# Performance work log

Measured on AMD Instinct MI355X. Metric: run time of the kernel, lower is better.

Reference implementation:

```python
import jax, jax.numpy as jnp
import numpy as np

NUM_NODES = 50000
NUM_EDGES = 800000
IN_CH = 64
OUT_CH = 64


def setup_inputs() -> dict:
    key = jax.random.key(0)
    k1, k2, k3, k4 = jax.random.split(key, 4)
    x = jax.random.normal(k1, (NUM_NODES, IN_CH), dtype=jnp.float32)
    edge_index = jax.random.randint(k2, (2, NUM_EDGES), 0, NUM_NODES, dtype=jnp.int32)
    W = jax.random.normal(k3, (IN_CH, OUT_CH), dtype=jnp.float32) * 0.05
    b = jax.random.normal(k4, (OUT_CH,), dtype=jnp.float32) * 0.05
    return {"x": x, "edge_index": edge_index, "W": W, "b": b}


def reference(x, edge_index, W, b):
    row, col = edge_index[0], edge_index[1]
    # Stage 1: in-degree of target nodes (math of one-hot sum == segment count)
    deg = jax.ops.segment_sum(jnp.ones_like(col, dtype=jnp.float32), col,
                              num_segments=NUM_NODES)
    deg_inv_sqrt = jnp.where(deg > 0, (deg + 1e-16) ** -0.5, 0.0)
    norm = deg_inv_sqrt[row] * deg_inv_sqrt[col]          # [E]
    # Stage 2+3: gather source features and scale by edge norm
    msg = norm[:, None] * x[row]                          # [E, IN_CH]
    # Stage 4: scatter-sum into target nodes (math of one-hot matmul)
    agg = jax.ops.segment_sum(msg, col, num_segments=NUM_NODES)  # [N, IN_CH]
    # Stage 5+6: linear transform + ReLU
    return jax.nn.relu(agg @ W + b)                       # [N, OUT_CH]
```

## Files before the change

### kernel.cpp

```cpp
#include <hip/hip_runtime.h>
#include <hip/hip_fp16.h>


#define C_CH 64
#define BW   128
#define BSH  7
#define MAXBUK 512
#define BIN_CHUNK 4096
#define NPB  32

__global__ void initcur_kernel(int* __restrict__ bcur, int nbuk, int cap) {
    int i = blockIdx.x * blockDim.x + threadIdx.x;
    if (i < nbuk) bcur[i] = i * cap;
}

__global__ void __launch_bounds__(256)
bin_kernel(const int* __restrict__ row, const int* __restrict__ col,
           int* __restrict__ bcur, unsigned* __restrict__ epk,
           int E, int nbuk, int cap) {
    __shared__ int h[MAXBUK];
    __shared__ int rb[MAXBUK];
    __shared__ unsigned short rank[BIN_CHUNK];
    int tid = threadIdx.x;
    int e0 = blockIdx.x * BIN_CHUNK;
    int cntE = E - e0; if (cntE > BIN_CHUNK) cntE = BIN_CHUNK;

    for (int i = tid; i < nbuk; i += 256) h[i] = 0;
    __syncthreads();

    const int4* col4 = (const int4*)(col + e0);
    const int4* row4 = (const int4*)(row + e0);
    int cnt4 = cntE >> 2;
    for (int i = tid; i < cnt4; i += 256) {
        int4 c = col4[i];
        rank[4*i+0] = (unsigned short)atomicAdd(&h[c.x >> BSH], 1);
        rank[4*i+1] = (unsigned short)atomicAdd(&h[c.y >> BSH], 1);
        rank[4*i+2] = (unsigned short)atomicAdd(&h[c.z >> BSH], 1);
        rank[4*i+3] = (unsigned short)atomicAdd(&h[c.w >> BSH], 1);
    }
    for (int i = (cnt4 << 2) + tid; i < cntE; i += 256)
        rank[i] = (unsigned short)atomicAdd(&h[col[e0 + i] >> BSH], 1);
    __syncthreads();

    for (int i = tid; i < nbuk; i += 256)
        rb[i] = h[i] ? atomicAdd(&bcur[i], h[i]) : 0;
    __syncthreads();

    for (int i = tid; i < cnt4; i += 256) {
        int4 c = col4[i];
        int4 r = row4[i];
        #pragma unroll
        for (int j = 0; j < 4; ++j) {
            int cc = (j == 0) ? c.x : (j == 1) ? c.y : (j == 2) ? c.z : c.w;
            int rr = (j == 0) ? r.x : (j == 1) ? r.y : (j == 2) ? r.z : r.w;
            int bkt = cc >> BSH;
            int pos = rb[bkt] + (int)rank[4*i+j];
            if (pos < (bkt + 1) * cap)
                epk[pos] = ((unsigned)(cc & (BW - 1)) << 16) | (unsigned)rr;
        }
    }
    for (int i = (cnt4 << 2) + tid; i < cntE; i += 256) {
        int cc = col[e0 + i];
        int bkt = cc >> BSH;
        int pos = rb[bkt] + (int)rank[i];
        if (pos < (bkt + 1) * cap)
            epk[pos] = ((unsigned)(cc & (BW - 1)) << 16) | (unsigned)row[e0 + i];
    }
}

__global__ void __launch_bounds__(256)
build_kernel(const unsigned* __restrict__ epk, const int* __restrict__ bcur,
             const float* __restrict__ x,
             int* __restrict__ rs, int* __restrict__ re, float* __restrict__ dis,
             unsigned short* __restrict__ srcs, __half* __restrict__ xsh,
             int N, int cap) {
    __shared__ int cnt[BW];
    __shared__ int sc[BW];
    __shared__ int cur[BW];
    __shared__ float dv[BW];
    __shared__ int tot;
    __shared__ unsigned short sl[4096];
    int tid = threadIdx.x;
    int b   = blockIdx.x;
    int base = b * cap;
    int cb = bcur[b] - base; if (cb > cap) cb = cap;
    int nb0 = b << BSH;
    int nn  = N - nb0; if (nn > BW) nn = BW;

    if (tid < BW) cnt[tid] = 0;
    for (int i = tid; i < cap; i += 256)
        sl[i] = (unsigned short)N;
    __syncthreads();
    for (int i = tid; i < cb; i += 256)
        atomicAdd(&cnt[epk[base + i] >> 16], 1);
    __syncthreads();
    if (tid < BW) sc[tid] = (cnt[tid] + 7) & ~7;
    __syncthreads();
    for (int off = 1; off < BW; off <<= 1) {
        int t = (tid < BW && tid >= off) ? sc[tid - off] : 0;
        __syncthreads();
        if (tid < BW) sc[tid] += t;
        __syncthreads();
    }
    if (tid < BW) {
        int d  = cnt[tid];
        int dp = (d + 7) & ~7;
        int ex = sc[tid] - dp;
        cur[tid] = ex;
        if (tid == BW - 1) tot = sc[tid];
        if (tid < nn) {
            rs[nb0 + tid] = base + ex;
            re[nb0 + tid] = base + ex + d;
            float di = (d > 0) ? rsqrtf((float)d) : 0.0f;
            dis[nb0 + tid] = di;
            dv[tid] = di;
        }
    }
    __syncthreads();
    for (int i = tid; i < cb; i += 256) {
        unsigned p = epk[base + i];
        int pos = atomicAdd(&cur[p >> 16], 1);
        if (pos < cap) sl[pos] = (unsigned short)(p & 0xFFFFu);
    }
    __syncthreads();
    int cbp = tot; if (cbp > cap) cbp = cap;
    for (int i = tid; i < cbp; i += 256)
        srcs[base + i] = sl[i];

    int tot2 = nn * (C_CH / 2);
    const float2* x2 = (const float2*)x;
    __half2* o2 = (__half2*)xsh;
    for (int i = tid; i < tot2; i += 256) {
        int nl = i >> 5;
        int c2 = i & 31;
        long long gi = (long long)(nb0 + nl) * (C_CH / 2) + c2;
        float2 v = x2[gi];
        float dn = dv[nl];
        o2[gi] = __floats2half2_rn(v.x * dn, v.y * dn);
    }
    if (b == 0 && tid < C_CH / 2)
        o2[(long long)N * (C_CH / 2) + tid] = __floats2half2_rn(0.0f, 0.0f);
}

__global__ void __launch_bounds__(512)
gather_kernel(const uint2* __restrict__ xsh8,
              const unsigned short* __restrict__ srcs,
              const int* __restrict__ rs, const int* __restrict__ re,
              const float* __restrict__ dis,
              const float* __restrict__ W, const float* __restrict__ b,
              float* __restrict__ out, int N) {
    __shared__ float Ws[C_CH * C_CH];
    __shared__ float bs[C_CH];
    __shared__ float ags[NPB][68];

    int tid = threadIdx.x;
    {
        const float4* W4 = (const float4*)W;
        float4* Ws4 = (float4*)Ws;
        for (int i = tid; i < C_CH * C_CH / 4; i += 512) Ws4[i] = W4[i];
        if (tid < C_CH) bs[tid] = b[tid];
    }

    int g  = tid >> 4;
    int c4 = tid & 15;
    int t = blockIdx.x * NPB + g;

    float4 acc = make_float4(0.f, 0.f, 0.f, 0.f);
    if (t < N) {
        int s0 = rs[t];
        int degp = ((re[t] - s0) + 7) & ~7;
        for (int eb = 0; eb < degp; eb += 8) {
            uint4 sv = *(const uint4*)(srcs + s0 + eb);
            int r0 = (int)(sv.x & 0xFFFFu), r1 = (int)(sv.x >> 16);
            int r2 = (int)(sv.y & 0xFFFFu), r3 = (int)(sv.y >> 16);
            int r4 = (int)(sv.z & 0xFFFFu), r5 = (int)(sv.z >> 16);
            int r6 = (int)(sv.w & 0xFFFFu), r7 = (int)(sv.w >> 16);
            uint2 u0 = xsh8[r0 * 16 + c4];
            uint2 u1 = xsh8[r1 * 16 + c4];
            uint2 u2 = xsh8[r2 * 16 + c4];
            uint2 u3 = xsh8[r3 * 16 + c4];
            uint2 u4 = xsh8[r4 * 16 + c4];
            uint2 u5 = xsh8[r5 * 16 + c4];
            uint2 u6 = xsh8[r6 * 16 + c4];
            uint2 u7 = xsh8[r7 * 16 + c4];
            #pragma unroll
            for (int k = 0; k < 8; ++k) {
                uint2 u = (k==0)?u0:(k==1)?u1:(k==2)?u2:(k==3)?u3:
                          (k==4)?u4:(k==5)?u5:(k==6)?u6:u7;
                float2 f0 = __half22float2(*(__half2*)&u.x);
                float2 f1 = __half22float2(*(__half2*)&u.y);
                acc.x += f0.x; acc.y += f0.y; acc.z += f1.x; acc.w += f1.y;
            }
        }
        float dt = dis[t];
        acc.x *= dt; acc.y *= dt; acc.z *= dt; acc.w *= dt;
        *(float4*)&ags[g][4 * c4] = acc;
    }
    __syncthreads();

    if (t < N) {
        float4 o = *(const float4*)&bs[4 * c4];
        #pragma unroll
        for (int kq = 0; kq < C_CH / 4; ++kq) {
            float4 a4 = *(const float4*)&ags[g][4 * kq];
            float4 w0 = *(const float4*)&Ws[(4 * kq + 0) * C_CH + 4 * c4];
            float4 w1 = *(const float4*)&Ws[(4 * kq + 1) * C_CH + 4 * c4];
            float4 w2 = *(const float4*)&Ws[(4 * kq + 2) * C_CH + 4 * c4];
            float4 w3 = *(const float4*)&Ws[(4 * kq + 3) * C_CH + 4 * c4];
            o.x = fmaf(a4.x, w0.x, o.x); o.y = fmaf(a4.x, w0.y, o.y);
            o.z = fmaf(a4.x, w0.z, o.z); o.w = fmaf(a4.x, w0.w, o.w);
            o.x = fmaf(a4.y, w1.x, o.x); o.y = fmaf(a4.y, w1.y, o.y);
            o.z = fmaf(a4.y, w1.z, o.z); o.w = fmaf(a4.y, w1.w, o.w);
            o.x = fmaf(a4.z, w2.x, o.x); o.y = fmaf(a4.z, w2.y, o.y);
            o.z = fmaf(a4.z, w2.z, o.z); o.w = fmaf(a4.z, w2.w, o.w);
            o.x = fmaf(a4.w, w3.x, o.x); o.y = fmaf(a4.w, w3.y, o.y);
            o.z = fmaf(a4.w, w3.z, o.z); o.w = fmaf(a4.w, w3.w, o.w);
        }
        o.x = fmaxf(o.x, 0.f); o.y = fmaxf(o.y, 0.f);
        o.z = fmaxf(o.z, 0.f); o.w = fmaxf(o.w, 0.f);
        *(float4*)&out[(long long)t * C_CH + 4 * c4] = o;
    }
}

extern "C" void kernel_launch(void* const* d_in, const int* in_sizes, int n_in,
                              void* d_out, int out_size, void* d_ws, size_t ws_size,
                              hipStream_t stream) {
    const float* x  = (const float*)d_in[0];
    const int*   ei = (const int*)  d_in[1];
    const float* W  = (const float*)d_in[2];
    const float* b  = (const float*)d_in[3];
    float* out = (float*)d_out;

    const int N = in_sizes[0] / C_CH;
    const int E = in_sizes[1] / 2;
    const int* row = ei;
    const int* col = ei + E;
    const int nbuk = (N + BW - 1) >> BSH;

    auto need = [&](int cap) {
        return (size_t)nbuk * cap * 6
             + (size_t)N * 12 + 256
             + (size_t)nbuk * 4
             + (size_t)(N + 1) * C_CH * 2;
    };
    int cap = 4096;
    if (ws_size < need(4096)) cap = 3072;

    char* ws = (char*)d_ws;
    unsigned* epk = (unsigned*)ws;      ws += (size_t)nbuk * cap * 4;
    unsigned short* srcs = (unsigned short*)ws;  ws += (size_t)nbuk * cap * 2;
    int* rs   = (int*)ws;               ws += (size_t)N * 4;
    int* re   = (int*)ws;               ws += (size_t)N * 4;
    float* dis = (float*)ws;            ws += (size_t)N * 4;
    int* bcur = (int*)ws;               ws += (size_t)nbuk * 4;
    __half* xsh = (__half*)ws;

    initcur_kernel<<<(nbuk + 255) / 256, 256, 0, stream>>>(bcur, nbuk, cap);
    bin_kernel <<<(E + BIN_CHUNK - 1) / BIN_CHUNK, 256, 0, stream>>>(row, col, bcur, epk, E, nbuk, cap);
    build_kernel<<<nbuk, 256, 0, stream>>>(epk, bcur, x, rs, re, dis, srcs, xsh, N, cap);
    gather_kernel<<<(N + NPB - 1) / NPB, 512, 0, stream>>>((const uint2*)xsh, srcs, rs, re,
                                                           dis, W, b, out, N);
}
```

Measured before the change: 60.26 us.

## Pack per-node segment metadata into int4, halve bin chunk, widen build blocks

Merges the separate row-start, row-end and inverse-sqrt-degree arrays into a single int4 per node, so the gather kernel does one 16-byte load instead of three scalar loads. Bucket cursors now start at zero and store relative offsets. The bin chunk size is halved to launch more bin blocks, and the build kernel moves from 256 to 512 threads. Together these aim to cut metadata traffic and raise parallelism in the binning and build stages, at the cost of more global atomics on the bucket counters.

```diff
diff --git a/kernel.cpp b/kernel.cpp
--- a/kernel.cpp
+++ b/kernel.cpp
@@ -6,12 +6,12 @@
 #define BW   128
 #define BSH  7
 #define MAXBUK 512
-#define BIN_CHUNK 4096
+#define BIN_CHUNK 2048
 #define NPB  32
 
-__global__ void initcur_kernel(int* __restrict__ bcur, int nbuk, int cap) {
+__global__ void clearcur_kernel(int* __restrict__ bcur, int nbuk) {
     int i = blockIdx.x * blockDim.x + threadIdx.x;
-    if (i < nbuk) bcur[i] = i * cap;
+    if (i < nbuk) bcur[i] = 0;
 }
 
 __global__ void __launch_bounds__(256)
@@ -54,24 +54,24 @@
             int cc = (j == 0) ? c.x : (j == 1) ? c.y : (j == 2) ? c.z : c.w;
             int rr = (j == 0) ? r.x : (j == 1) ? r.y : (j == 2) ? r.z : r.w;
             int bkt = cc >> BSH;
-            int pos = rb[bkt] + (int)rank[4*i+j];
-            if (pos < (bkt + 1) * cap)
-                epk[pos] = ((unsigned)(cc & (BW - 1)) << 16) | (unsigned)rr;
+            int rel = rb[bkt] + (int)rank[4*i+j];
+            if (rel < cap)
+                epk[bkt * cap + rel] = ((unsigned)(cc & (BW - 1)) << 16) | (unsigned)rr;
         }
     }
     for (int i = (cnt4 << 2) + tid; i < cntE; i += 256) {
         int cc = col[e0 + i];
         int bkt = cc >> BSH;
-        int pos = rb[bkt] + (int)rank[i];
-        if (pos < (bkt + 1) * cap)
-            epk[pos] = ((unsigned)(cc & (BW - 1)) << 16) | (unsigned)row[e0 + i];
-    }
-}
-
-__global__ void __launch_bounds__(256)
+        int rel = rb[bkt] + (int)rank[i];
+        if (rel < cap)
+            epk[bkt * cap + rel] = ((unsigned)(cc & (BW - 1)) << 16) | (unsigned)row[e0 + i];
+    }
+}
+
+__global__ void __launch_bounds__(512)
 build_kernel(const unsigned* __restrict__ epk, const int* __restrict__ bcur,
              const float* __restrict__ x,
-             int* __restrict__ rs, int* __restrict__ re, float* __restrict__ dis,
+             int4* __restrict__ seg,
              unsigned short* __restrict__ srcs, __half* __restrict__ xsh,
              int N, int cap) {
     __shared__ int cnt[BW];
@@ -83,15 +83,15 @@
     int tid = threadIdx.x;
     int b   = blockIdx.x;
     int base = b * cap;
-    int cb = bcur[b] - base; if (cb > cap) cb = cap;
+    int cb = bcur[b]; if (cb > cap) cb = cap;
     int nb0 = b << BSH;
     int nn  = N - nb0; if (nn > BW) nn = BW;
 
     if (tid < BW) cnt[tid] = 0;
-    for (int i = tid; i < cap; i += 256)
+    for (int i = tid; i < cap; i += 512)
         sl[i] = (unsigned short)N;
     __syncthreads();
-    for (int i = tid; i < cb; i += 256)
+    for (int i = tid; i < cb; i += 512)
         atomicAdd(&cnt[epk[base + i] >> 16], 1);
     __syncthreads();
     if (tid < BW) sc[tid] = (cnt[tid] + 7) & ~7;
@@ -109,28 +109,26 @@
         cur[tid] = ex;
         if (tid == BW - 1) tot = sc[tid];
         if (tid < nn) {
-            rs[nb0 + tid] = base + ex;
-            re[nb0 + tid] = base + ex + d;
             float di = (d > 0) ? rsqrtf((float)d) : 0.0f;
-            dis[nb0 + tid] = di;
             dv[tid] = di;
-        }
-    }
-    __syncthreads();
-    for (int i = tid; i < cb; i += 256) {
+            seg[nb0 + tid] = make_int4(base + ex, d, __float_as_int(di), 0);
+        }
+    }
+    __syncthreads();
+    for (int i = tid; i < cb; i += 512) {
         unsigned p = epk[base + i];
         int pos = atomicAdd(&cur[p >> 16], 1);
         if (pos < cap) sl[pos] = (unsigned short)(p & 0xFFFFu);
     }
     __syncthreads();
     int cbp = tot; if (cbp > cap) cbp = cap;
-    for (int i = tid; i < cbp; i += 256)
+    for (int i = tid; i < cbp; i += 512)
         srcs[base + i] = sl[i];
 
     int tot2 = nn * (C_CH / 2);
     const float2* x2 = (const float2*)x;
     __half2* o2 = (__half2*)xsh;
-    for (int i = tid; i < tot2; i += 256) {
+    for (int i = tid; i < tot2; i += 512) {
         int nl = i >> 5;
         int c2 = i & 31;
         long long gi = (long long)(nb0 + nl) * (C_CH / 2) + c2;
@@ -145,8 +143,7 @@
 __global__ void __launch_bounds__(512)
 gather_kernel(const uint2* __restrict__ xsh8,
               const unsigned short* __restrict__ srcs,
-              const int* __restrict__ rs, const int* __restrict__ re,
-              const float* __restrict__ dis,
+              const int4* __restrict__ seg,
               const float* __restrict__ W, const float* __restrict__ b,
               float* __restrict__ out, int N) {
     __shared__ float Ws[C_CH * C_CH];
@@ -165,10 +162,11 @@
     int c4 = tid & 15;
     int t = blockIdx.x * NPB + g;
 
-    float4 acc = make_float4(0.f, 0.f, 0.f, 0.f);
     if (t < N) {
-        int s0 = rs[t];
-        int degp = ((re[t] - s0) + 7) & ~7;
+        float4 acc = make_float4(0.f, 0.f, 0.f, 0.f);
+        int4 sg = seg[t];
+        int s0 = sg.x;
+        int degp = (sg.y + 7) & ~7;
         for (int eb = 0; eb < degp; eb += 8) {
             uint4 sv = *(const uint4*)(srcs + s0 + eb);
             int r0 = (int)(sv.x & 0xFFFFu), r1 = (int)(sv.x >> 16);
@@ -192,7 +190,7 @@
                 acc.x += f0.x; acc.y += f0.y; acc.z += f1.x; acc.w += f1.y;
             }
         }
-        float dt = dis[t];
+        float dt = __int_as_float(sg.z);
         acc.x *= dt; acc.y *= dt; acc.z *= dt; acc.w *= dt;
         *(float4*)&ags[g][4 * c4] = acc;
     }
@@ -239,7 +237,7 @@
 
     auto need = [&](int cap) {
         return (size_t)nbuk * cap * 6
-             + (size_t)N * 12 + 256
+             + (size_t)N * 16 + 256
              + (size_t)nbuk * 4
              + (size_t)(N + 1) * C_CH * 2;
     };
@@ -249,15 +247,13 @@
     char* ws = (char*)d_ws;
     unsigned* epk = (unsigned*)ws;      ws += (size_t)nbuk * cap * 4;
     unsigned short* srcs = (unsigned short*)ws;  ws += (size_t)nbuk * cap * 2;
-    int* rs   = (int*)ws;               ws += (size_t)N * 4;
-    int* re   = (int*)ws;               ws += (size_t)N * 4;
-    float* dis = (float*)ws;            ws += (size_t)N * 4;
+    int4* seg = (int4*)ws;              ws += (size_t)N * 16;
     int* bcur = (int*)ws;               ws += (size_t)nbuk * 4;
     __half* xsh = (__half*)ws;
 
-    initcur_kernel<<<(nbuk + 255) / 256, 256, 0, stream>>>(bcur, nbuk, cap);
+    clearcur_kernel<<<(nbuk + 255) / 256, 256, 0, stream>>>(bcur, nbuk);
     bin_kernel <<<(E + BIN_CHUNK - 1) / BIN_CHUNK, 256, 0, stream>>>(row, col, bcur, epk, E, nbuk, cap);
-    build_kernel<<<nbuk, 256, 0, stream>>>(epk, bcur, x, rs, re, dis, srcs, xsh, N, cap);
-    gather_kernel<<<(N + NPB - 1) / NPB, 512, 0, stream>>>((const uint2*)xsh, srcs, rs, re,
-                                                           dis, W, b, out, N);
-}
+    build_kernel<<<nbuk, 512, 0, stream>>>(epk, bcur, x, seg, srcs, xsh, N, cap);
+    gather_kernel<<<(N + NPB - 1) / NPB, 512, 0, stream>>>((const uint2*)xsh, srcs, seg,
+                                                           W, b, out, N);
+}
```

Measured after the change: 58.99 us. 1.02x faster.
